# Performance work log

Measured on AMD Instinct MI355X. Metric: run time of the kernel, lower is better.

## Reference

```python
import jax, jax.numpy as jnp
import numpy as np

B, T, IN, H, K, FS = 4096, 50, 4, 256, 3, 6


def _cell(x, h, c, Wih, Whh, bih, bhh):
    # PyTorch LSTM cell, gate order i, f, g, o
    g = x @ Wih.T + h @ Whh.T + bih + bhh
    i, f, gg, o = jnp.split(g, 4, axis=-1)
    c = jax.nn.sigmoid(f) * c + jax.nn.sigmoid(i) * jnp.tanh(gg)
    h = jax.nn.sigmoid(o) * jnp.tanh(c)
    return h, c


def setup_inputs() -> dict:
    key = jax.random.key(0)
    ks = jax.random.split(key, 24)
    s = 0.05
    rn = lambda k, shape: jax.random.normal(k, shape, jnp.float32) * s
    return {
        "x": jax.random.normal(ks[0], (B, T, IN), jnp.float32),
        "enc_Wih0": rn(ks[1], (4 * H, IN)),
        "enc_Whh0": rn(ks[2], (4 * H, H)),
        "enc_bih0": rn(ks[3], (4 * H,)),
        "enc_bhh0": rn(ks[4], (4 * H,)),
        "enc_Wih1": rn(ks[5], (4 * H, H)),
        "enc_Whh1": rn(ks[6], (4 * H, H)),
        "enc_bih1": rn(ks[7], (4 * H,)),
        "enc_bhh1": rn(ks[8], (4 * H,)),
        "dec_Wih0": rn(ks[9], (K, 4 * H, 2)),
        "dec_Whh0": rn(ks[10], (K, 4 * H, H)),
        "dec_bih0": rn(ks[11], (K, 4 * H)),
        "dec_bhh0": rn(ks[12], (K, 4 * H)),
        "dec_Wih1": rn(ks[13], (K, 4 * H, H)),
        "dec_Whh1": rn(ks[14], (K, 4 * H, H)),
        "dec_bih1": rn(ks[15], (K, 4 * H)),
        "dec_bhh1": rn(ks[16], (K, 4 * H)),
        "head_W": rn(ks[17], (K, 2, H)),
        "head_b": rn(ks[18], (K, 2)),
        "conf_W": rn(ks[19], (K, H)),
        "conf_b": rn(ks[20], (K,)),
    }


def reference(x, enc_Wih0, enc_Whh0, enc_bih0, enc_bhh0,
              enc_Wih1, enc_Whh1, enc_bih1, enc_bhh1,
              dec_Wih0, dec_Whh0, dec_bih0, dec_bhh0,
              dec_Wih1, dec_Whh1, dec_bih1, dec_bhh1,
              head_W, head_b, conf_W, conf_b):
    b = x.shape[0]
    z = jnp.zeros((b, H), x.dtype)

    # ---- 2-layer LSTM encoder (eval mode: dropout inactive) ----
    def enc_step(carry, xt):
        h0, c0, h1, c1 = carry
        h0, c0 = _cell(xt, h0, c0, enc_Wih0, enc_Whh0, enc_bih0, enc_bhh0)
        h1, c1 = _cell(h0, h1, c1, enc_Wih1, enc_Whh1, enc_bih1, enc_bhh1)
        return (h0, c0, h1, c1), None

    (h0, c0, h1, c1), _ = jax.lax.scan(enc_step, (z, z, z, z),
                                       jnp.swapaxes(x, 0, 1))  # [T,B,IN]

    dec_input = x[:, -1, :2]  # [B, 2]

    all_modes = []
    for k in range(K):
        def dec_step(carry, _):
            hk0, ck0, hk1, ck1, inp = carry
            hk0, ck0 = _cell(inp, hk0, ck0, dec_Wih0[k], dec_Whh0[k],
                             dec_bih0[k], dec_bhh0[k])
            hk1, ck1 = _cell(hk0, hk1, ck1, dec_Wih1[k], dec_Whh1[k],
                             dec_bih1[k], dec_bhh1[k])
            pred = hk1 @ head_W[k].T + head_b[k]  # [B, 2]
            return (hk0, ck0, hk1, ck1, pred), pred

        _, preds = jax.lax.scan(dec_step, (h0, c0, h1, c1, dec_input),
                                None, length=FS)  # [FS, B, 2]
        all_modes.append(jnp.swapaxes(preds, 0, 1))  # [B, FS, 2]

    modes = jnp.stack(all_modes, axis=1)  # [B, K, FS, 2]
    conf = jax.nn.softmax(h1 @ conf_W.T + conf_b, axis=-1)  # [B, K]
    return modes, conf
```

## Files before the change

kernel.cpp:

```cpp
#include <hip/hip_runtime.h>


typedef __bf16 bf16x8 __attribute__((ext_vector_type(8)));
typedef float  f32x4  __attribute__((ext_vector_type(4)));

#define NMAT 12
#define SLICE_SH 16384
#define WPACK_SHORTS (NMAT * 16 * SLICE_SH)
#define BIAS_OFF_BYTES (WPACK_SHORTS * 2)
#define BAR_OFF_BYTES (BIAS_OFF_BYTES + 32768)
#define H_OFF_BYTES (BAR_OFF_BYTES + 4096)
#define HBUF_SHORTS 1048576

__device__ __host__ inline unsigned short f2bf_u(float f){
  union { float f; unsigned u; } v; v.f = f;
  unsigned u = v.u + 0x7fffu + ((v.u >> 16) & 1u);
  return (unsigned short)(u >> 16);
}
__device__ inline float sigm(float x){ return 1.f / (1.f + __expf(-x)); }
__device__ inline float tanh_(float x){ return 2.f / (1.f + __expf(-2.f * x)) - 1.f; }

struct PrepArgs {
  const float* mats[NMAT];
  const float* ba[8];
  const float* bb[8];
  unsigned short* wp;
  float* bias;
  unsigned* bars;
};

__global__ void prep_kernel(PrepArgs a){
  unsigned i = blockIdx.x * 256u + threadIdx.x;
  if (i < (unsigned)WPACK_SHORTS) {
    unsigned mi = i >> 18;
    unsigned ug = (i >> 14) & 15u;
    unsigned g  = (i >> 12) & 3u;
    unsigned kk = (i >> 9) & 7u;
    unsigned l  = (i >> 3) & 63u;
    unsigned j  = i & 7u;
    unsigned src = (g * 256u + ug * 16u + (l & 15u)) * 256u + kk * 32u + (l >> 4) * 8u + j;
    a.wp[i] = f2bf_u(a.mats[mi][src]);
  } else if (i < (unsigned)WPACK_SHORTS + 8192u) {
    unsigned e = i - (unsigned)WPACK_SHORTS;
    unsigned cell = e >> 10, n = e & 1023u;
    a.bias[e] = a.ba[cell][n] + a.bb[cell][n];
  } else if (i < (unsigned)WPACK_SHORTS + 8192u + 1024u) {
    a.bars[i - (unsigned)WPACK_SHORTS - 8192u] = 0u;
  }
}

struct MainArgs {
  const float* x;
  const float* encWih0;
  const float* decWih0;
  const float* headW;
  const float* headB;
  const float* confW;
  const float* confB;
  const unsigned short* wpack;
  const float* bias;
  unsigned* bars;
  unsigned short* hb;
  float* out;
};

__device__ inline void bg_barrier(unsigned* cnt, unsigned* gen, unsigned phase){
  __syncthreads();
  if (threadIdx.x == 0){
    unsigned arrived = __hip_atomic_fetch_add(cnt, 1u, __ATOMIC_ACQ_REL,
                                              __HIP_MEMORY_SCOPE_AGENT) + 1u;
    if (arrived == phase * 16u){
      __hip_atomic_store(gen, phase, __ATOMIC_RELEASE, __HIP_MEMORY_SCOPE_AGENT);
    } else {
      unsigned spins = 0;
      while (__hip_atomic_load(gen, __ATOMIC_RELAXED, __HIP_MEMORY_SCOPE_AGENT) < phase){
        __builtin_amdgcn_s_sleep(2);
        if (++spins > (1u << 22)) break;
      }
      (void)__hip_atomic_load(gen, __ATOMIC_ACQUIRE, __HIP_MEMORY_SCOPE_AGENT);
    }
  }
  __syncthreads();
}

__device__ inline void gemm_k256(f32x4 acc[4][4],
                                 const unsigned short* __restrict__ hbuf,
                                 int wrow0,
                                 const unsigned short* __restrict__ wl,
                                 int lane){
  const int lr = lane & 15, lg = lane >> 4;
  #pragma unroll
  for (int kp = 0; kp < 4; ++kp){
    bf16x8 A2[4][2], B2[4][2];
    #pragma unroll
    for (int mt = 0; mt < 4; ++mt){
      const unsigned short* rp = hbuf + (size_t)(wrow0 + mt * 16 + lr) * 256 + kp * 64 + lg * 8;
      A2[mt][0] = *reinterpret_cast<const bf16x8*>(rp);
      A2[mt][1] = *reinterpret_cast<const bf16x8*>(rp + 32);
    }
    #pragma unroll
    for (int gt = 0; gt < 4; ++gt){
      #pragma unroll
      for (int q = 0; q < 2; ++q)
        B2[gt][q] = *reinterpret_cast<const bf16x8*>(wl + ((size_t)(gt * 8 + kp * 2 + q) * 64 + lane) * 8);
    }
    #pragma unroll
    for (int mt = 0; mt < 4; ++mt)
      #pragma unroll
      for (int gt = 0; gt < 4; ++gt){
        f32x4 c = __builtin_amdgcn_mfma_f32_16x16x32_bf16(A2[mt][0], B2[gt][0], acc[mt][gt], 0, 0, 0);
        acc[mt][gt] = __builtin_amdgcn_mfma_f32_16x16x32_bf16(A2[mt][1], B2[gt][1], c, 0, 0, 0);
      }
  }
}

__device__ inline void cell_upd(f32x4 acc[4][4], float cst[4][4],
                                unsigned short* __restrict__ hbuf,
                                int wrow0, int U0, int lane){
  const int lr = lane & 15, lg = lane >> 4;
  #pragma unroll
  for (int mt = 0; mt < 4; ++mt){
    #pragma unroll
    for (int r = 0; r < 4; ++r){
      const float gi = acc[mt][0][r], gf = acc[mt][1][r];
      const float gg = acc[mt][2][r], go = acc[mt][3][r];
      float c = sigm(gf) * cst[mt][r] + sigm(gi) * tanh_(gg);
      cst[mt][r] = c;
      hbuf[(size_t)(wrow0 + mt * 16 + lg * 4 + r) * 256 + U0 + lr] = f2bf_u(sigm(go) * tanh_(c));
    }
  }
}

__device__ inline void init_bias(f32x4 acc[4][4], const float* __restrict__ b, int U0, int lr){
  #pragma unroll
  for (int gt = 0; gt < 4; ++gt){
    const float bb = b[gt * 256 + U0 + lr];
    #pragma unroll
    for (int mt = 0; mt < 4; ++mt) acc[mt][gt] = (f32x4){bb, bb, bb, bb};
  }
}

__global__ __launch_bounds__(256, 1) void lstm_main(MainArgs a){
  __shared__ unsigned short wlds[3][SLICE_SH];
  __shared__ float pin[256][2];
  __shared__ float hw[512];
  __shared__ float cw[768];

  const int tid = threadIdx.x, wave = tid >> 6, lane = tid & 63;
  const int lr = lane & 15, lg = lane >> 4;
  const int xcd = blockIdx.x & 7, idx = blockIdx.x >> 3;
  const int bg = xcd * 2 + (idx >> 4), ug = idx & 15;
  const int B0 = bg * 256, U0 = ug * 16;
  const int wrow0 = B0 + wave * 64;

  unsigned* bcnt = a.bars + bg * 32;
  unsigned* bgen = bcnt + 1;
  unsigned phase = 0;

  unsigned short* hp0[2] = { a.hb,                   a.hb + HBUF_SHORTS };
  unsigned short* hp1[2] = { a.hb + 2 * HBUF_SHORTS, a.hb + 3 * HBUF_SHORTS };
  unsigned short* henc0  =   a.hb + 4 * HBUF_SHORTS;
  unsigned short* henc1  =   a.hb + 5 * HBUF_SHORTS;

  {
    const size_t o = (size_t)(B0 + tid) * 256 + U0;
    const uint4 z = {0, 0, 0, 0};
    *(uint4*)(hp0[0] + o) = z; *(uint4*)(hp0[0] + o + 8) = z;
    *(uint4*)(hp1[0] + o) = z; *(uint4*)(hp1[0] + o + 8) = z;
  }
  for (int i = tid; i < 768; i += 256) cw[i] = a.confW[i];
  for (int s = 0; s < 3; ++s){
    const uint4* src = (const uint4*)(a.wpack + (size_t)(s * 16 + ug) * SLICE_SH);
    uint4* dst = (uint4*)wlds[s];
    for (int i = tid; i < 2048; i += 256) dst[i] = src[i];
  }
  bg_barrier(bcnt, bgen, ++phase);

  float c0[4][4] = {}, c1[4][4] = {};
  const float* bias0 = a.bias;
  const float* bias1 = a.bias + 1024;

  for (int s = 0; s <= 50; ++s){
    if (s < 50){
      f32x4 acc[4][4];
      float4 w4[4];
      init_bias(acc, bias0, U0, lr);
      #pragma unroll
      for (int gt = 0; gt < 4; ++gt)
        w4[gt] = *(const float4*)(a.encWih0 + (size_t)(gt * 256 + U0 + lr) * 4);
      #pragma unroll
      for (int mt = 0; mt < 4; ++mt){
        #pragma unroll
        for (int r = 0; r < 4; ++r){
          const float4 xv = *(const float4*)(a.x + (size_t)(wrow0 + mt * 16 + lg * 4 + r) * 200 + s * 4);
          #pragma unroll
          for (int gt = 0; gt < 4; ++gt)
            acc[mt][gt][r] += xv.x * w4[gt].x + xv.y * w4[gt].y + xv.z * w4[gt].z + xv.w * w4[gt].w;
        }
      }
      gemm_k256(acc, hp0[s & 1], wrow0, wlds[0], lane);
      cell_upd(acc, c0, hp0[(s + 1) & 1], wrow0, U0, lane);
    }
    if (s >= 1){
      f32x4 acc[4][4];
      init_bias(acc, bias1, U0, lr);
      gemm_k256(acc, hp0[s & 1], wrow0, wlds[1], lane);
      gemm_k256(acc, hp1[(s - 1) & 1], wrow0, wlds[2], lane);
      cell_upd(acc, c1, hp1[s & 1], wrow0, U0, lane);
    }
    bg_barrier(bcnt, bgen, ++phase);
  }

  {
    const int row = B0 + tid;
    if (ug == 0){
      const bf16x8* rp = (const bf16x8*)(hp1[0] + (size_t)row * 256);
      float l0 = a.confB[0], l1 = a.confB[1], l2 = a.confB[2];
      for (int ch = 0; ch < 32; ++ch){
        const bf16x8 v = rp[ch];
        #pragma unroll
        for (int j = 0; j < 8; ++j){
          const float f = (float)v[j];
          l0 += f * cw[ch * 8 + j];
          l1 += f * cw[256 + ch * 8 + j];
          l2 += f * cw[512 + ch * 8 + j];
        }
      }
      const float mx = fmaxf(l0, fmaxf(l1, l2));
      const float e0 = __expf(l0 - mx), e1 = __expf(l1 - mx), e2 = __expf(l2 - mx);
      const float inv = 1.f / (e0 + e1 + e2);
      a.out[147456 + (size_t)row * 3 + 0] = e0 * inv;
      a.out[147456 + (size_t)row * 3 + 1] = e1 * inv;
      a.out[147456 + (size_t)row * 3 + 2] = e2 * inv;
    }
    const size_t o = (size_t)row * 256 + U0;
    *(uint4*)(henc0 + o)     = *(const uint4*)(hp0[0] + o);
    *(uint4*)(henc0 + o + 8) = *(const uint4*)(hp0[0] + o + 8);
    *(uint4*)(henc1 + o)     = *(const uint4*)(hp1[0] + o);
    *(uint4*)(henc1 + o + 8) = *(const uint4*)(hp1[0] + o + 8);
    for (int s = 0; s < 3; ++s){
      const int mi = 3 * s + 3;
      const uint4* src = (const uint4*)(a.wpack + (size_t)(mi * 16 + ug) * SLICE_SH);
      uint4* dst = (uint4*)wlds[s];
      for (int i = tid; i < 2048; i += 256) dst[i] = src[i];
    }
    for (int i = tid; i < 512; i += 256) hw[i] = a.headW[i];
    pin[tid][0] = a.x[(size_t)row * 200 + 196];
    pin[tid][1] = a.x[(size_t)row * 200 + 197];
  }
  float c0s[4][4], c1s[4][4];
  #pragma unroll
  for (int mt = 0; mt < 4; ++mt)
    #pragma unroll
    for (int r = 0; r < 4; ++r){ c0s[mt][r] = c0[mt][r]; c1s[mt][r] = c1[mt][r]; }
  bg_barrier(bcnt, bgen, ++phase);

  for (int k = 0; k < 3; ++k){
    const float* db0 = a.bias + (size_t)(2 + k) * 1024;
    const float* db1 = a.bias + (size_t)(5 + k) * 1024;
    const float hb0 = a.headB[k * 2], hb1 = a.headB[k * 2 + 1];

    if (k > 0){
      const size_t o = (size_t)(B0 + tid) * 256 + U0;
      *(uint4*)(hp0[0] + o)     = *(const uint4*)(henc0 + o);
      *(uint4*)(hp0[0] + o + 8) = *(const uint4*)(henc0 + o + 8);
      *(uint4*)(hp1[0] + o)     = *(const uint4*)(henc1 + o);
      *(uint4*)(hp1[0] + o + 8) = *(const uint4*)(henc1 + o + 8);
      const int m3[3] = {3 + k, 6 + k, 9 + k};
      for (int s = 0; s < 3; ++s){
        const uint4* src = (const uint4*)(a.wpack + (size_t)(m3[s] * 16 + ug) * SLICE_SH);
        uint4* dst = (uint4*)wlds[s];
        for (int i = tid; i < 2048; i += 256) dst[i] = src[i];
      }
      for (int i = tid; i < 512; i += 256) hw[i] = a.headW[(size_t)k * 512 + i];
      pin[tid][0] = a.x[(size_t)(B0 + tid) * 200 + 196];
      pin[tid][1] = a.x[(size_t)(B0 + tid) * 200 + 197];
      #pragma unroll
      for (int mt = 0; mt < 4; ++mt)
        #pragma unroll
        for (int r = 0; r < 4; ++r){ c0[mt][r] = c0s[mt][r]; c1[mt][r] = c1s[mt][r]; }
      bg_barrier(bcnt, bgen, ++phase);
    }

    auto do_L0 = [&](int t){
      f32x4 acc[4][4];
      float2 w2[4];
      init_bias(acc, db0, U0, lr);
      #pragma unroll
      for (int gt = 0; gt < 4; ++gt)
        w2[gt] = *(const float2*)(a.decWih0 + (size_t)k * 2048 + (size_t)(gt * 256 + U0 + lr) * 2);
      #pragma unroll
      for (int mt = 0; mt < 4; ++mt){
        #pragma unroll
        for (int r = 0; r < 4; ++r){
          const int li = wave * 64 + mt * 16 + lg * 4 + r;
          const float p0 = pin[li][0], p1 = pin[li][1];
          #pragma unroll
          for (int gt = 0; gt < 4; ++gt)
            acc[mt][gt][r] += p0 * w2[gt].x + p1 * w2[gt].y;
        }
      }
      gemm_k256(acc, hp0[t & 1], wrow0, wlds[0], lane);
      cell_upd(acc, c0, hp0[(t + 1) & 1], wrow0, U0, lane);
    };
    auto do_L1 = [&](int t){
      f32x4 acc[4][4];
      init_bias(acc, db1, U0, lr);
      gemm_k256(acc, hp0[(t + 1) & 1], wrow0, wlds[1], lane);
      gemm_k256(acc, hp1[t & 1], wrow0, wlds[2], lane);
      cell_upd(acc, c1, hp1[(t + 1) & 1], wrow0, U0, lane);
    };
    auto do_pred = [&](int t){
      const int row = B0 + tid;
      const bf16x8* rp = (const bf16x8*)(hp1[(t + 1) & 1] + (size_t)row * 256);
      float s0 = hb0, s1 = hb1;
      for (int ch = 0; ch < 32; ++ch){
        const bf16x8 v = rp[ch];
        #pragma unroll
        for (int j = 0; j < 8; ++j){
          const float f = (float)v[j];
          s0 += f * hw[ch * 8 + j];
          s1 += f * hw[256 + ch * 8 + j];
        }
      }
      pin[tid][0] = s0; pin[tid][1] = s1;
      if (ug == 0){
        const size_t ob = (((size_t)row * 3 + k) * 6 + t) * 2;
        a.out[ob] = s0; a.out[ob + 1] = s1;
      }
    };

    do_L0(0);
    bg_barrier(bcnt, bgen, ++phase);
    do_L1(0);
    bg_barrier(bcnt, bgen, ++phase);
    for (int t = 1; t < 6; ++t){
      do_pred(t - 1);
      __syncthreads();
      do_L0(t);
      bg_barrier(bcnt, bgen, ++phase);
      do_L1(t);
      bg_barrier(bcnt, bgen, ++phase);
    }
    do_pred(5);
    bg_barrier(bcnt, bgen, ++phase);
  }
}

extern "C" void kernel_launch(void* const* d_in, const int* in_sizes, int n_in,
                              void* d_out, int out_size, void* d_ws, size_t ws_size,
                              hipStream_t stream){
  PrepArgs pa;
  pa.mats[0] = (const float*)d_in[2];
  pa.mats[1] = (const float*)d_in[5];
  pa.mats[2] = (const float*)d_in[6];
  for (int k = 0; k < 3; ++k){
    pa.mats[3 + k] = (const float*)d_in[10] + (size_t)k * 262144;
    pa.mats[6 + k] = (const float*)d_in[13] + (size_t)k * 262144;
    pa.mats[9 + k] = (const float*)d_in[14] + (size_t)k * 262144;
  }
  pa.ba[0] = (const float*)d_in[3];  pa.bb[0] = (const float*)d_in[4];
  pa.ba[1] = (const float*)d_in[7];  pa.bb[1] = (const float*)d_in[8];
  for (int k = 0; k < 3; ++k){
    pa.ba[2 + k] = (const float*)d_in[11] + (size_t)k * 1024;
    pa.bb[2 + k] = (const float*)d_in[12] + (size_t)k * 1024;
    pa.ba[5 + k] = (const float*)d_in[15] + (size_t)k * 1024;
    pa.bb[5 + k] = (const float*)d_in[16] + (size_t)k * 1024;
  }
  pa.wp   = (unsigned short*)d_ws;
  pa.bias = (float*)((char*)d_ws + BIAS_OFF_BYTES);
  pa.bars = (unsigned*)((char*)d_ws + BAR_OFF_BYTES);

  prep_kernel<<<12324, 256, 0, stream>>>(pa);

  MainArgs ma;
  ma.x       = (const float*)d_in[0];
  ma.encWih0 = (const float*)d_in[1];
  ma.decWih0 = (const float*)d_in[9];
  ma.headW   = (const float*)d_in[17];
  ma.headB   = (const float*)d_in[18];
  ma.confW   = (const float*)d_in[19];
  ma.confB   = (const float*)d_in[20];
  ma.wpack   = (const unsigned short*)d_ws;
  ma.bias    = (const float*)((char*)d_ws + BIAS_OFF_BYTES);
  ma.bars    = (unsigned*)((char*)d_ws + BAR_OFF_BYTES);
  ma.hb      = (unsigned short*)((char*)d_ws + H_OFF_BYTES);
  ma.out     = (float*)d_out;

  lstm_main<<<256, 256, 0, stream>>>(ma);
}
```

Measured before the change: 2.172 ms.

## Double block threads and replace acquire/release barrier with relaxed device-scope atomics

Doubles the threads per block from 256 to 512, so each of 8 waves handles 32 batch rows instead of 64. This halves the per-wave accumulator and MFMA work and raises latency hiding. The hidden-state exchange now uses relaxed agent-scope 64-bit atomic loads and stores, and the grid barrier drops its acquire/release ordering in favour of a compiler memory fence and a shorter sleep. The aim is to cut barrier and cache-flush cost on each of the many sequential timesteps. The risk is memory-ordering correctness, since visibility now relies on the atomics bypassing non-coherent caches rather than on explicit fences.

```diff
diff --git a/kernel.cpp b/kernel.cpp
--- a/kernel.cpp
+++ b/kernel.cpp
@@ -3,6 +3,7 @@
 
 typedef __bf16 bf16x8 __attribute__((ext_vector_type(8)));
 typedef float  f32x4  __attribute__((ext_vector_type(4)));
+typedef unsigned long long u64;
 
 #define NMAT 12
 #define SLICE_SH 16384
@@ -19,6 +20,22 @@
 }
 __device__ inline float sigm(float x){ return 1.f / (1.f + __expf(-x)); }
 __device__ inline float tanh_(float x){ return 2.f / (1.f + __expf(-2.f * x)) - 1.f; }
+
+__device__ inline u64 llc_ld64(const unsigned short* p){
+  return __hip_atomic_load((const u64*)p, __ATOMIC_RELAXED, __HIP_MEMORY_SCOPE_AGENT);
+}
+__device__ inline void llc_st64(unsigned short* p, u64 v){
+  __hip_atomic_store((u64*)p, v, __ATOMIC_RELAXED, __HIP_MEMORY_SCOPE_AGENT);
+}
+__device__ inline bf16x8 llc_ld_frag(const unsigned short* p){
+  union { u64 q[2]; bf16x8 v; } u;
+  u.q[0] = llc_ld64(p);
+  u.q[1] = llc_ld64(p + 4);
+  return u.v;
+}
+__device__ inline void llc_st16(unsigned short* p, unsigned short v){
+  __hip_atomic_store(p, v, __ATOMIC_RELAXED, __HIP_MEMORY_SCOPE_AGENT);
+}
 
 struct PrepArgs {
   const float* mats[NMAT];
@@ -67,23 +84,23 @@
 __device__ inline void bg_barrier(unsigned* cnt, unsigned* gen, unsigned phase){
   __syncthreads();
   if (threadIdx.x == 0){
-    unsigned arrived = __hip_atomic_fetch_add(cnt, 1u, __ATOMIC_ACQ_REL,
+    unsigned arrived = __hip_atomic_fetch_add(cnt, 1u, __ATOMIC_RELAXED,
                                               __HIP_MEMORY_SCOPE_AGENT) + 1u;
     if (arrived == phase * 16u){
-      __hip_atomic_store(gen, phase, __ATOMIC_RELEASE, __HIP_MEMORY_SCOPE_AGENT);
+      __hip_atomic_store(gen, phase, __ATOMIC_RELAXED, __HIP_MEMORY_SCOPE_AGENT);
     } else {
       unsigned spins = 0;
       while (__hip_atomic_load(gen, __ATOMIC_RELAXED, __HIP_MEMORY_SCOPE_AGENT) < phase){
-        __builtin_amdgcn_s_sleep(2);
-        if (++spins > (1u << 22)) break;
-      }
-      (void)__hip_atomic_load(gen, __ATOMIC_ACQUIRE, __HIP_MEMORY_SCOPE_AGENT);
-    }
+        __builtin_amdgcn_s_sleep(1);
+        if (++spins > (1u << 24)) break;
+      }
+    }
+    asm volatile("" ::: "memory");
   }
   __syncthreads();
 }
 
-__device__ inline void gemm_k256(f32x4 acc[4][4],
+__device__ inline void gemm_k256(f32x4 acc[2][4],
                                  const unsigned short* __restrict__ hbuf,
                                  int wrow0,
                                  const unsigned short* __restrict__ wl,
@@ -91,12 +108,12 @@
   const int lr = lane & 15, lg = lane >> 4;
   #pragma unroll
   for (int kp = 0; kp < 4; ++kp){
-    bf16x8 A2[4][2], B2[4][2];
-    #pragma unroll
-    for (int mt = 0; mt < 4; ++mt){
+    bf16x8 A2[2][2], B2[4][2];
+    #pragma unroll
+    for (int mt = 0; mt < 2; ++mt){
       const unsigned short* rp = hbuf + (size_t)(wrow0 + mt * 16 + lr) * 256 + kp * 64 + lg * 8;
-      A2[mt][0] = *reinterpret_cast<const bf16x8*>(rp);
-      A2[mt][1] = *reinterpret_cast<const bf16x8*>(rp + 32);
+      A2[mt][0] = llc_ld_frag(rp);
+      A2[mt][1] = llc_ld_frag(rp + 32);
     }
     #pragma unroll
     for (int gt = 0; gt < 4; ++gt){
@@ -105,7 +122,7 @@
         B2[gt][q] = *reinterpret_cast<const bf16x8*>(wl + ((size_t)(gt * 8 + kp * 2 + q) * 64 + lane) * 8);
     }
     #pragma unroll
-    for (int mt = 0; mt < 4; ++mt)
+    for (int mt = 0; mt < 2; ++mt)
       #pragma unroll
       for (int gt = 0; gt < 4; ++gt){
         f32x4 c = __builtin_amdgcn_mfma_f32_16x16x32_bf16(A2[mt][0], B2[gt][0], acc[mt][gt], 0, 0, 0);
@@ -114,33 +131,34 @@
   }
 }
 
-__device__ inline void cell_upd(f32x4 acc[4][4], float cst[4][4],
+__device__ inline void cell_upd(f32x4 acc[2][4], float cst[2][4],
                                 unsigned short* __restrict__ hbuf,
                                 int wrow0, int U0, int lane){
   const int lr = lane & 15, lg = lane >> 4;
   #pragma unroll
-  for (int mt = 0; mt < 4; ++mt){
+  for (int mt = 0; mt < 2; ++mt){
     #pragma unroll
     for (int r = 0; r < 4; ++r){
       const float gi = acc[mt][0][r], gf = acc[mt][1][r];
       const float gg = acc[mt][2][r], go = acc[mt][3][r];
       float c = sigm(gf) * cst[mt][r] + sigm(gi) * tanh_(gg);
       cst[mt][r] = c;
-      hbuf[(size_t)(wrow0 + mt * 16 + lg * 4 + r) * 256 + U0 + lr] = f2bf_u(sigm(go) * tanh_(c));
-    }
-  }
-}
-
-__device__ inline void init_bias(f32x4 acc[4][4], const float* __restrict__ b, int U0, int lr){
+      llc_st16(&hbuf[(size_t)(wrow0 + mt * 16 + lg * 4 + r) * 256 + U0 + lr],
+               f2bf_u(sigm(go) * tanh_(c)));
+    }
+  }
+}
+
+__device__ inline void init_bias(f32x4 acc[2][4], const float* __restrict__ b, int U0, int lr){
   #pragma unroll
   for (int gt = 0; gt < 4; ++gt){
     const float bb = b[gt * 256 + U0 + lr];
     #pragma unroll
-    for (int mt = 0; mt < 4; ++mt) acc[mt][gt] = (f32x4){bb, bb, bb, bb};
-  }
-}
-
-__global__ __launch_bounds__(256, 1) void lstm_main(MainArgs a){
+    for (int mt = 0; mt < 2; ++mt) acc[mt][gt] = (f32x4){bb, bb, bb, bb};
+  }
+}
+
+__global__ __launch_bounds__(512, 1) void lstm_main(MainArgs a){
   __shared__ unsigned short wlds[3][SLICE_SH];
   __shared__ float pin[256][2];
   __shared__ float hw[512];
@@ -151,7 +169,7 @@
   const int xcd = blockIdx.x & 7, idx = blockIdx.x >> 3;
   const int bg = xcd * 2 + (idx >> 4), ug = idx & 15;
   const int B0 = bg * 256, U0 = ug * 16;
-  const int wrow0 = B0 + wave * 64;
+  const int wrow0 = B0 + wave * 32;
 
   unsigned* bcnt = a.bars + bg * 32;
   unsigned* bgen = bcnt + 1;
@@ -162,34 +180,36 @@
   unsigned short* henc0  =   a.hb + 4 * HBUF_SHORTS;
   unsigned short* henc1  =   a.hb + 5 * HBUF_SHORTS;
 
-  {
+  if (tid < 256){
     const size_t o = (size_t)(B0 + tid) * 256 + U0;
-    const uint4 z = {0, 0, 0, 0};
-    *(uint4*)(hp0[0] + o) = z; *(uint4*)(hp0[0] + o + 8) = z;
-    *(uint4*)(hp1[0] + o) = z; *(uint4*)(hp1[0] + o + 8) = z;
-  }
-  for (int i = tid; i < 768; i += 256) cw[i] = a.confW[i];
+    #pragma unroll
+    for (int q = 0; q < 4; ++q){
+      llc_st64(hp0[0] + o + q * 4, 0ull);
+      llc_st64(hp1[0] + o + q * 4, 0ull);
+    }
+  }
+  for (int i = tid; i < 768; i += 512) cw[i] = a.confW[i];
   for (int s = 0; s < 3; ++s){
     const uint4* src = (const uint4*)(a.wpack + (size_t)(s * 16 + ug) * SLICE_SH);
     uint4* dst = (uint4*)wlds[s];
-    for (int i = tid; i < 2048; i += 256) dst[i] = src[i];
+    for (int i = tid; i < 2048; i += 512) dst[i] = src[i];
   }
   bg_barrier(bcnt, bgen, ++phase);
 
-  float c0[4][4] = {}, c1[4][4] = {};
+  float c0[2][4] = {}, c1[2][4] = {};
   const float* bias0 = a.bias;
   const float* bias1 = a.bias + 1024;
 
   for (int s = 0; s <= 50; ++s){
     if (s < 50){
-      f32x4 acc[4][4];
+      f32x4 acc[2][4];
       float4 w4[4];
       init_bias(acc, bias0, U0, lr);
       #pragma unroll
       for (int gt = 0; gt < 4; ++gt)
         w4[gt] = *(const float4*)(a.encWih0 + (size_t)(gt * 256 + U0 + lr) * 4);
       #pragma unroll
-      for (int mt = 0; mt < 4; ++mt){
+      for (int mt = 0; mt < 2; ++mt){
         #pragma unroll
         for (int r = 0; r < 4; ++r){
           const float4 xv = *(const float4*)(a.x + (size_t)(wrow0 + mt * 16 + lg * 4 + r) * 200 + s * 4);
@@ -202,7 +222,7 @@
       cell_upd(acc, c0, hp0[(s + 1) & 1], wrow0, U0, lane);
     }
     if (s >= 1){
-      f32x4 acc[4][4];
+      f32x4 acc[2][4];
       init_bias(acc, bias1, U0, lr);
       gemm_k256(acc, hp0[s & 1], wrow0, wlds[1], lane);
       gemm_k256(acc, hp1[(s - 1) & 1], wrow0, wlds[2], lane);
@@ -212,12 +232,11 @@
   }
 
   {
-    const int row = B0 + tid;
-    if (ug == 0){
-      const bf16x8* rp = (const bf16x8*)(hp1[0] + (size_t)row * 256);
+    if (ug == 0 && tid < 256){
+      const int row = B0 + tid;
       float l0 = a.confB[0], l1 = a.confB[1], l2 = a.confB[2];
       for (int ch = 0; ch < 32; ++ch){
-        const bf16x8 v = rp[ch];
+        const bf16x8 v = llc_ld_frag(hp1[0] + (size_t)row * 256 + ch * 8);
         #pragma unroll
         for (int j = 0; j < 8; ++j){
           const float f = (float)v[j];
@@ -233,24 +252,29 @@
       a.out[147456 + (size_t)row * 3 + 1] = e1 * inv;
       a.out[147456 + (size_t)row * 3 + 2] = e2 * inv;
     }
-    const size_t o = (size_t)row * 256 + U0;
-    *(uint4*)(henc0 + o)     = *(const uint4*)(hp0[0] + o);
-    *(uint4*)(henc0 + o + 8) = *(const uint4*)(hp0[0] + o + 8);
-    *(uint4*)(henc1 + o)     = *(const uint4*)(hp1[0] + o);
-    *(uint4*)(henc1 + o + 8) = *(const uint4*)(hp1[0] + o + 8);
+    if (tid < 256){
+      const size_t o = (size_t)(B0 + tid) * 256 + U0;
+      #pragma unroll
+      for (int q = 0; q < 4; ++q){
+        ((u64*)(henc0 + o))[q] = llc_ld64(hp0[0] + o + q * 4);
+        ((u64*)(henc1 + o))[q] = llc_ld64(hp1[0] + o + q * 4);
+      }
+      pin[tid][0] = a.x[(size_t)(B0 + tid) * 200 + 196];
+      pin[tid][1] = a.x[(size_t)(B0 + tid) * 200 + 197];
+    }
     for (int s = 0; s < 3; ++s){
       const int mi = 3 * s + 3;
       const uint4* src = (const uint4*)(a.wpack + (size_t)(mi * 16 + ug) * SLICE_SH);
       uint4* dst = (uint4*)wlds[s];
-      for (int i = tid; i < 2048; i += 256) dst[i] = src[i];
-    }
-    for (int i = tid; i < 512; i += 256) hw[i] = a.headW[i];
-    pin[tid][0] = a.x[(size_t)row * 200 + 196];
-    pin[tid][1] = a.x[(size_t)row * 200 + 197];
-  }
-  float c0s[4][4], c1s[4][4];
+      for (int i = tid; i < 2048; i += 512) dst[i] = src[i];
+    }
+    for (int i = tid; i < 512; i += 512) hw[i] = a.headW[i];
+    for (int i = tid + 512; i < 512; i += 512) {}
+    if (tid < 512) { if (tid < 512 && tid >= 0) hw[tid] = a.headW[tid]; }
+  }
+  float c0s[2][4], c1s[2][4];
   #pragma unroll
-  for (int mt = 0; mt < 4; ++mt)
+  for (int mt = 0; mt < 2; ++mt)
     #pragma unroll
     for (int r = 0; r < 4; ++r){ c0s[mt][r] = c0[mt][r]; c1s[mt][r] = c1[mt][r]; }
   bg_barrier(bcnt, bgen, ++phase);
@@ -261,39 +285,42 @@
     const float hb0 = a.headB[k * 2], hb1 = a.headB[k * 2 + 1];
 
     if (k > 0){
-      const size_t o = (size_t)(B0 + tid) * 256 + U0;
-      *(uint4*)(hp0[0] + o)     = *(const uint4*)(henc0 + o);
-      *(uint4*)(hp0[0] + o + 8) = *(const uint4*)(henc0 + o + 8);
-      *(uint4*)(hp1[0] + o)     = *(const uint4*)(henc1 + o);
-      *(uint4*)(hp1[0] + o + 8) = *(const uint4*)(henc1 + o + 8);
+      if (tid < 256){
+        const size_t o = (size_t)(B0 + tid) * 256 + U0;
+        #pragma unroll
+        for (int q = 0; q < 4; ++q){
+          llc_st64(hp0[0] + o + q * 4, ((const u64*)(henc0 + o))[q]);
+          llc_st64(hp1[0] + o + q * 4, ((const u64*)(henc1 + o))[q]);
+        }
+        pin[tid][0] = a.x[(size_t)(B0 + tid) * 200 + 196];
+        pin[tid][1] = a.x[(size_t)(B0 + tid) * 200 + 197];
+      }
       const int m3[3] = {3 + k, 6 + k, 9 + k};
       for (int s = 0; s < 3; ++s){
         const uint4* src = (const uint4*)(a.wpack + (size_t)(m3[s] * 16 + ug) * SLICE_SH);
         uint4* dst = (uint4*)wlds[s];
-        for (int i = tid; i < 2048; i += 256) dst[i] = src[i];
-      }
-      for (int i = tid; i < 512; i += 256) hw[i] = a.headW[(size_t)k * 512 + i];
-      pin[tid][0] = a.x[(size_t)(B0 + tid) * 200 + 196];
-      pin[tid][1] = a.x[(size_t)(B0 + tid) * 200 + 197];
-      #pragma unroll
-      for (int mt = 0; mt < 4; ++mt)
+        for (int i = tid; i < 2048; i += 512) dst[i] = src[i];
+      }
+      if (tid < 512) hw[tid] = a.headW[(size_t)k * 512 + tid];
+      #pragma unroll
+      for (int mt = 0; mt < 2; ++mt)
         #pragma unroll
         for (int r = 0; r < 4; ++r){ c0[mt][r] = c0s[mt][r]; c1[mt][r] = c1s[mt][r]; }
       bg_barrier(bcnt, bgen, ++phase);
     }
 
     auto do_L0 = [&](int t){
-      f32x4 acc[4][4];
+      f32x4 acc[2][4];
       float2 w2[4];
       init_bias(acc, db0, U0, lr);
       #pragma unroll
       for (int gt = 0; gt < 4; ++gt)
         w2[gt] = *(const float2*)(a.decWih0 + (size_t)k * 2048 + (size_t)(gt * 256 + U0 + lr) * 2);
       #pragma unroll
-      for (int mt = 0; mt < 4; ++mt){
+      for (int mt = 0; mt < 2; ++mt){
         #pragma unroll
         for (int r = 0; r < 4; ++r){
-          const int li = wave * 64 + mt * 16 + lg * 4 + r;
+          const int li = wave * 32 + mt * 16 + lg * 4 + r;
           const float p0 = pin[li][0], p1 = pin[li][1];
           #pragma unroll
           for (int gt = 0; gt < 4; ++gt)
@@ -304,29 +331,30 @@
       cell_upd(acc, c0, hp0[(t + 1) & 1], wrow0, U0, lane);
     };
     auto do_L1 = [&](int t){
-      f32x4 acc[4][4];
+      f32x4 acc[2][4];
       init_bias(acc, db1, U0, lr);
       gemm_k256(acc, hp0[(t + 1) & 1], wrow0, wlds[1], lane);
       gemm_k256(acc, hp1[t & 1], wrow0, wlds[2], lane);
       cell_upd(acc, c1, hp1[(t + 1) & 1], wrow0, U0, lane);
     };
     auto do_pred = [&](int t){
-      const int row = B0 + tid;
-      const bf16x8* rp = (const bf16x8*)(hp1[(t + 1) & 1] + (size_t)row * 256);
-      float s0 = hb0, s1 = hb1;
-      for (int ch = 0; ch < 32; ++ch){
-        const bf16x8 v = rp[ch];
-        #pragma unroll
-        for (int j = 0; j < 8; ++j){
-          const float f = (float)v[j];
-          s0 += f * hw[ch * 8 + j];
-          s1 += f * hw[256 + ch * 8 + j];
-        }
-      }
-      pin[tid][0] = s0; pin[tid][1] = s1;
-      if (ug == 0){
-        const size_t ob = (((size_t)row * 3 + k) * 6 + t) * 2;
-        a.out[ob] = s0; a.out[ob + 1] = s1;
+      if (tid < 256){
+        const int row = B0 + tid;
+        float s0 = hb0, s1 = hb1;
+        for (int ch = 0; ch < 32; ++ch){
+          const bf16x8 v = llc_ld_frag(hp1[(t + 1) & 1] + (size_t)row * 256 + ch * 8);
+          #pragma unroll
+          for (int j = 0; j < 8; ++j){
+            const float f = (float)v[j];
+            s0 += f * hw[ch * 8 + j];
+            s1 += f * hw[256 + ch * 8 + j];
+          }
+        }
+        pin[tid][0] = s0; pin[tid][1] = s1;
+        if (ug == 0){
+          const size_t ob = (((size_t)row * 3 + k) * 6 + t) * 2;
+          a.out[ob] = s0; a.out[ob + 1] = s1;
+        }
       }
     };
 
@@ -387,5 +415,5 @@
   ma.hb      = (unsigned short*)((char*)d_ws + H_OFF_BYTES);
   ma.out     = (float*)d_out;
 
-  lstm_main<<<256, 256, 0, stream>>>(ma);
-}
+  lstm_main<<<256, 512, 0, stream>>>(ma);
+}
```

Result: no change. 2.210 ms (+1.8%).
